# Kernel tuning notes

Hardware: AMD Instinct MI355X
Metric: run time of the kernel (lower is better)

The kernel has to match this reference:

```python
import jax, jax.numpy as jnp
import numpy as np

B, SQ, SK, D, H, DH = 4, 1024, 1024, 1024, 16, 64  # transform_units*head_units == 1024


def setup_inputs() -> dict:
    key = jax.random.key(0)
    ks = jax.random.split(key, 8)
    q = jax.random.normal(ks[0], (B, SQ, D), dtype=jnp.float32)
    v = jax.random.normal(ks[1], (B, SK, D), dtype=jnp.float32)
    q_mask = jax.random.randint(ks[2], (B, SQ), 0, 2).astype(bool).at[:, 0].set(True)
    v_mask = jax.random.randint(ks[3], (B, SK), 0, 2).astype(bool).at[:, 0].set(True)
    s = 0.02
    Wq = jax.random.normal(ks[4], (D, H * DH), dtype=jnp.float32) * s
    Wk = jax.random.normal(ks[5], (D, H * DH), dtype=jnp.float32) * s
    Wv = jax.random.normal(ks[6], (D, H * DH), dtype=jnp.float32) * s
    Wo = jax.random.normal(ks[7], (H * DH, D), dtype=jnp.float32) * s
    bq = jnp.zeros((H * DH,), jnp.float32)
    bk = jnp.zeros((H * DH,), jnp.float32)
    bv = jnp.zeros((H * DH,), jnp.float32)
    bo = jnp.zeros((D,), jnp.float32)
    return {"q": q, "v": v, "q_mask": q_mask, "v_mask": v_mask,
            "Wq": Wq, "bq": bq, "Wk": Wk, "bk": bk, "Wv": Wv, "bv": bv,
            "Wo": Wo, "bo": bo}


def reference(q, v, q_mask, v_mask, Wq, bq, Wk, bk, Wv, bv, Wo, bo):
    # k = v in the original module
    k = v
    # QKV projections; split-last-dim + batch-concat trick == reshape to heads
    Q = (q @ Wq + bq).reshape(B, SQ, H, DH)
    Kh = (k @ Wk + bk).reshape(B, SK, H, DH)
    V = (v @ Wv + bv).reshape(B, SK, H, DH)
    # Keras Attention: unscaled dot-product scores
    scores = jnp.einsum('bqhd,bkhd->bhqk', Q, Kh)  # [B,H,SQ,SK]
    scores = jnp.where(v_mask[:, None, None, :], scores, jnp.float32(-1e9))
    attn = jax.nn.softmax(scores, axis=-1)
    ctx = jnp.einsum('bhqk,bkhd->bqhd', attn, V).reshape(B, SQ, H * DH)
    # Keras Attention zeros masked query positions before output dense
    ctx = ctx * q_mask[:, :, None].astype(ctx.dtype)
    return ctx @ Wo + bo
```

## Files before the change

### kernel.cpp

```cpp
#include <hip/hip_runtime.h>
#include <hip/hip_fp16.h>

typedef __attribute__((ext_vector_type(8))) _Float16 f16x8;
typedef __attribute__((ext_vector_type(4))) float f32x4;

__device__ __forceinline__ void gload_lds16(const _Float16* g, _Float16* l) {
  __builtin_amdgcn_global_load_lds((const __attribute__((address_space(1))) void*)g,
                                   (__attribute__((address_space(3))) void*)l, 16, 0, 0);
}

__global__ __launch_bounds__(256) void prep_kernel(
    const float* __restrict__ q, const float* __restrict__ v,
    const float* __restrict__ W0, const float* __restrict__ W1,
    const float* __restrict__ W2, const float* __restrict__ W3,
    _Float16* __restrict__ q16, _Float16* __restrict__ v16,
    _Float16* __restrict__ T0, _Float16* __restrict__ T1,
    _Float16* __restrict__ T2, _Float16* __restrict__ T3) {
  __shared__ float tile[64 * 65];
  int tid = threadIdx.x, ybl = blockIdx.y;
  if (ybl < 16) {
    int i = (ybl * 256 + blockIdx.x) * 256 + tid;
    float4 fq = ((const float4*)q)[i];
    float4 fv = ((const float4*)v)[i];
    union { _Float16 h[4]; uint2 u; } oq, ov;
    oq.h[0] = (_Float16)fq.x; oq.h[1] = (_Float16)fq.y;
    oq.h[2] = (_Float16)fq.z; oq.h[3] = (_Float16)fq.w;
    ov.h[0] = (_Float16)fv.x; ov.h[1] = (_Float16)fv.y;
    ov.h[2] = (_Float16)fv.z; ov.h[3] = (_Float16)fv.w;
    *(uint2*)&q16[4 * (size_t)i] = oq.u;
    *(uint2*)&v16[4 * (size_t)i] = ov.u;
    return;
  }
  int z = ybl - 16;
  const float* W = (z == 0) ? W0 : (z == 1) ? W1 : (z == 2) ? W2 : W3;
  _Float16* T = (z == 0) ? T0 : (z == 1) ? T1 : (z == 2) ? T2 : T3;
  int bx = (blockIdx.x & 15) * 64, by = (blockIdx.x >> 4) * 64;
  for (int it = 0; it < 4; it++) {
    int lin = it * 256 + tid;
    int r = lin >> 4, q4 = (lin & 15) * 4;
    float4 f = *(const float4*)&W[(size_t)(by + r) * 1024 + bx + q4];
    tile[r * 65 + q4 + 0] = f.x;
    tile[r * 65 + q4 + 1] = f.y;
    tile[r * 65 + q4 + 2] = f.z;
    tile[r * 65 + q4 + 3] = f.w;
  }
  __syncthreads();
  for (int it = 0; it < 2; it++) {
    int lin = it * 256 + tid;
    int orow = lin >> 3, seg = (lin & 7) * 8;
    union { uint4 u; _Float16 h[8]; } o;
    for (int e = 0; e < 8; e++) o.h[e] = (_Float16)tile[(seg + e) * 65 + orow];
    *(uint4*)&T[(size_t)(bx + orow) * 1024 + by + seg] = o.u;
  }
}

__global__ __launch_bounds__(256, 3) void gemm_qkv_kernel(
    const _Float16* __restrict__ q16, const _Float16* __restrict__ v16,
    const _Float16* __restrict__ WqT, const _Float16* __restrict__ WkT,
    const _Float16* __restrict__ WvT,
    const float* __restrict__ bq, const float* __restrict__ bk, const float* __restrict__ bv,
    _Float16* __restrict__ Q16, _Float16* __restrict__ K16, _Float16* __restrict__ VT16) {
  int ord = blockIdx.x + (blockIdx.y << 3) + (blockIdx.z << 8);
  int wgid = (ord & 7) * 96 + (ord >> 3);
  int z = wgid >> 8;
  int rem = wgid & 255;
  int m0 = (rem >> 3) * 128, n0 = (rem & 7) * 128;

  const _Float16* A = (z == 0) ? q16 : v16;
  const _Float16* BT = (z == 0) ? WqT : ((z == 1) ? WkT : WvT);
  const float* bias = (z == 0) ? bq : ((z == 1) ? bk : bv);
  const int K = 1024;

  __shared__ _Float16 Alds[2][128 * 32];
  __shared__ _Float16 Blds[2][128 * 32];
  int tid = threadIdx.x, lane = tid & 63, w = tid >> 6;
  int c = lane & 15, g = lane >> 4;
  int wm = (w & 1) * 64, wn = (w >> 1) * 64;
  int rr = lane >> 2;
  int su = ((lane & 3) ^ (rr & 3)) * 8;

  const _Float16* gA[2]; const _Float16* gB[2]; int lo[2];
  for (int p = 0; p < 2; p++) {
    int row = w * 32 + p * 16 + rr;
    gA[p] = &A[(size_t)(m0 + row) * K + su];
    gB[p] = &BT[(size_t)(n0 + row) * K + su];
    lo[p] = (w * 32 + p * 16) * 32;
  }

  f32x4 acc[4][4];
  for (int i = 0; i < 4; i++)
    for (int j = 0; j < 4; j++)
      acc[i][j] = (f32x4){0.f, 0.f, 0.f, 0.f};

  for (int p = 0; p < 2; p++) {
    gload_lds16(gA[p], &Alds[0][lo[p]]);
    gload_lds16(gB[p], &Blds[0][lo[p]]);
  }
  __syncthreads();

  int xa = (c & 3) << 4;
  int cur = 0;
  for (int kt = 0; kt < 32; kt++) {
    if (kt + 1 < 32) {
      int nb = cur ^ 1;
      for (int p = 0; p < 2; p++) {
        gload_lds16(gA[p] + (kt + 1) * 32, &Alds[nb][lo[p]]);
        gload_lds16(gB[p] + (kt + 1) * 32, &Blds[nb][lo[p]]);
      }
    }
    const char* ab = (const char*)&Alds[cur][0];
    const char* bb = (const char*)&Blds[cur][0];
    f16x8 af[4], bf[4];
    for (int i = 0; i < 4; i++)
      af[i] = *(const f16x8*)(ab + (wm + i * 16 + c) * 64 + ((g * 16) ^ xa));
    for (int j = 0; j < 4; j++)
      bf[j] = *(const f16x8*)(bb + (wn + j * 16 + c) * 64 + ((g * 16) ^ xa));
    for (int i = 0; i < 4; i++)
      for (int j = 0; j < 4; j++)
        acc[i][j] = __builtin_amdgcn_mfma_f32_16x16x32_f16(af[i], bf[j], acc[i][j], 0, 0, 0);
    __syncthreads();
    cur ^= 1;
  }

  if (z < 2) {
    _Float16* C = (z == 0) ? Q16 : K16;
    for (int j = 0; j < 4; j++) {
      float bv_ = bias[n0 + wn + j * 16 + c];
      for (int i = 0; i < 4; i++) {
        int r = m0 + wm + i * 16 + g * 4;
        int cc = n0 + wn + j * 16 + c;
        for (int e = 0; e < 4; e++)
          C[(size_t)(r + e) * 1024 + cc] = (_Float16)(acc[i][j][e] + bv_);
      }
    }
  } else {
    for (int j = 0; j < 4; j++) {
      int cc = n0 + wn + j * 16 + c;
      float bv_ = bias[cc];
      int h_ = cc >> 6, dh = cc & 63;
      for (int i = 0; i < 4; i++) {
        int r = m0 + wm + i * 16 + g * 4;
        int b_ = r >> 10, key = r & 1023;
        union { uint2 u; _Float16 hh[4]; } o;
        for (int e = 0; e < 4; e++) o.hh[e] = (_Float16)(acc[i][j][e] + bv_);
        *(uint2*)&VT16[((size_t)((b_ * 16 + h_) * 64 + dh)) * 1024 + key] = o.u;
      }
    }
  }
}

__global__ __launch_bounds__(256, 2) void gemm_out_kernel(
    const _Float16* __restrict__ ctx16, const _Float16* __restrict__ WoT,
    const float* __restrict__ bo, float* __restrict__ out) {
  int ord = blockIdx.x + (blockIdx.y << 4);
  int wgid = (ord & 7) * 64 + (ord >> 3);
  int n0 = (wgid & 15) * 64, m0 = (wgid >> 4) * 128;
  const int K = 1024;
  __shared__ _Float16 Alds[2][128 * 32];
  __shared__ _Float16 Blds[2][64 * 32];
  int tid = threadIdx.x, lane = tid & 63, w = tid >> 6;
  int c = lane & 15, g = lane >> 4;
  int wm = (w & 1) * 64, wn = (w >> 1) * 32;
  int rr = lane >> 2;
  int su = ((lane & 3) ^ (rr & 3)) * 8;

  const _Float16* gA[2]; int laoff[2];
  for (int p = 0; p < 2; p++) {
    int row = w * 32 + p * 16 + rr;
    gA[p] = &ctx16[(size_t)(m0 + row) * K + su];
    laoff[p] = (w * 32 + p * 16) * 32;
  }
  const _Float16* gB; int lboff;
  {
    int row = w * 16 + rr;
    gB = &WoT[(size_t)(n0 + row) * K + su];
    lboff = (w * 16) * 32;
  }

  f32x4 acc[4][2];
  for (int i = 0; i < 4; i++)
    for (int j = 0; j < 2; j++)
      acc[i][j] = (f32x4){0.f, 0.f, 0.f, 0.f};

  for (int p = 0; p < 2; p++) gload_lds16(gA[p], &Alds[0][laoff[p]]);
  gload_lds16(gB, &Blds[0][lboff]);
  __syncthreads();

  int xa = (c & 3) << 4;
  int cur = 0;
  for (int kt = 0; kt < 32; kt++) {
    if (kt + 1 < 32) {
      int nb = cur ^ 1;
      for (int p = 0; p < 2; p++) gload_lds16(gA[p] + (kt + 1) * 32, &Alds[nb][laoff[p]]);
      gload_lds16(gB + (kt + 1) * 32, &Blds[nb][lboff]);
    }
    const char* ab = (const char*)&Alds[cur][0];
    const char* bb = (const char*)&Blds[cur][0];
    f16x8 af[4], bf[2];
    for (int i = 0; i < 4; i++)
      af[i] = *(const f16x8*)(ab + (wm + i * 16 + c) * 64 + ((g * 16) ^ xa));
    for (int j = 0; j < 2; j++)
      bf[j] = *(const f16x8*)(bb + (wn + j * 16 + c) * 64 + ((g * 16) ^ xa));
    for (int i = 0; i < 4; i++)
      for (int j = 0; j < 2; j++)
        acc[i][j] = __builtin_amdgcn_mfma_f32_16x16x32_f16(af[i], bf[j], acc[i][j], 0, 0, 0);
    __syncthreads();
    cur ^= 1;
  }
  for (int j = 0; j < 2; j++) {
    float bv_ = bo[n0 + wn + j * 16 + c];
    for (int i = 0; i < 4; i++) {
      int r = m0 + wm + i * 16 + g * 4;
      int cc = n0 + wn + j * 16 + c;
      for (int e = 0; e < 4; e++)
        out[(size_t)(r + e) * 1024 + cc] = acc[i][j][e] + bv_;
    }
  }
}

__global__ __launch_bounds__(256, 4) void attn_kernel(
    const _Float16* __restrict__ Q16, const _Float16* __restrict__ K16,
    const _Float16* __restrict__ VT16,
    const int* __restrict__ q_mask, const int* __restrict__ v_mask,
    _Float16* __restrict__ ctx16) {
  int ord = blockIdx.x + (blockIdx.y << 4) + (blockIdx.z << 8);
  int wgid = (ord & 7) * 128 + (ord >> 3);
  int qb = wgid & 15, h = (wgid >> 4) & 15, b = wgid >> 8;
  int tid = threadIdx.x, lane = tid & 63, w = tid >> 6;
  int c = lane & 15, g = lane >> 4;
  int lr = lane >> 3, ls = lane & 7;

  __shared__ _Float16 QP[64 * 64];
  __shared__ _Float16 Kl[2][64 * 64];
  __shared__ _Float16 Vl[2][64 * 64];

  const _Float16* Qg = Q16 + ((size_t)(b * 1024 + qb * 64)) * 1024 + h * 64;
  const _Float16* Kg = K16 + ((size_t)(b * 1024)) * 1024 + h * 64;
  const _Float16* Vg = VT16 + ((size_t)(b * 16 + h)) * 64 * 1024;

  int row0 = w * 16 + lr, row1 = row0 + 8;
  int kx = (ls ^ lr) * 8;
  int ch0 = w * 2, ch1 = w * 2 + 1;

  gload_lds16(Qg + (size_t)row0 * 1024 + kx, QP + ch0 * 512);
  gload_lds16(Qg + (size_t)row1 * 1024 + kx, QP + ch1 * 512);
  gload_lds16(Kg + (size_t)row0 * 1024 + kx, &Kl[0][ch0 * 512]);
  gload_lds16(Kg + (size_t)row1 * 1024 + kx, &Kl[0][ch1 * 512]);
  gload_lds16(Vg + (size_t)row0 * 1024 + kx, &Vl[0][ch0 * 512]);
  gload_lds16(Vg + (size_t)row1 * 1024 + kx, &Vl[0][ch1 * 512]);
  __syncthreads();

  f16x8 qf[2];
  {
    int row = w * 16 + c;
    const char* rb = (const char*)QP + row * 128;
    int x = (row & 7) << 4;
    qf[0] = *(const f16x8*)(rb + ((g * 16) ^ x));
    qf[1] = *(const f16x8*)(rb + ((64 + g * 16) ^ x));
    const _Float16 l2e = (_Float16)1.44269504f;
    for (int e = 0; e < 8; e++) { qf[0][e] *= l2e; qf[1][e] *= l2e; }
  }

  float lp[4] = {0.f, 0.f, 0.f, 0.f};
  f32x4 acc_o[4];
  for (int jd = 0; jd < 4; jd++) acc_o[jd] = (f32x4){0.f, 0.f, 0.f, 0.f};

  char* pb = (char*)QP;
  int cur = 0;
  const float REF = -23.0831222f;
  for (int kb = 0; kb < 16; kb++) {
    if (kb + 1 < 16) {
      int nb = cur ^ 1;
      const _Float16* kgs = Kg + (size_t)(kb + 1) * 64 * 1024;
      const _Float16* vgs = Vg + (kb + 1) * 64;
      gload_lds16(kgs + (size_t)row0 * 1024 + kx, &Kl[nb][ch0 * 512]);
      gload_lds16(kgs + (size_t)row1 * 1024 + kx, &Kl[nb][ch1 * 512]);
      gload_lds16(vgs + (size_t)row0 * 1024 + kx, &Vl[nb][ch0 * 512]);
      gload_lds16(vgs + (size_t)row1 * 1024 + kx, &Vl[nb][ch1 * 512]);
    }
    float madd[4];
    for (int j = 0; j < 4; j++)
      madd[j] = v_mask[b * 1024 + kb * 64 + j * 16 + c] ? REF : -1e30f;

    f32x4 s[4];
    const char* kbse = (const char*)&Kl[cur][0];
    for (int j = 0; j < 4; j++) {
      int row = j * 16 + c;
      const char* rb = kbse + row * 128;
      int x = (row & 7) << 4;
      f16x8 k0 = *(const f16x8*)(rb + ((g * 16) ^ x));
      f16x8 k1 = *(const f16x8*)(rb + ((64 + g * 16) ^ x));
      s[j] = (f32x4){0.f, 0.f, 0.f, 0.f};
      s[j] = __builtin_amdgcn_mfma_f32_16x16x32_f16(qf[0], k0, s[j], 0, 0, 0);
      s[j] = __builtin_amdgcn_mfma_f32_16x16x32_f16(qf[1], k1, s[j], 0, 0, 0);
    }

    for (int j = 0; j < 4; j++)
      for (int e = 0; e < 4; e++) {
        float p = exp2f(s[j][e] + madd[j]);
        s[j][e] = p;
        lp[e] += p;
      }

    for (int j = 0; j < 4; j++)
      for (int e = 0; e < 4; e++) {
        int prow = w * 16 + g * 4 + e;
        int pby = prow * 128 + (((j * 16 + c) * 2) ^ ((prow & 7) << 4));
        *(_Float16*)(pb + pby) = (_Float16)s[j][e];
      }
    asm volatile("s_waitcnt lgkmcnt(0)" ::: "memory");
    __builtin_amdgcn_sched_barrier(0);

    const char* vbse = (const char*)&Vl[cur][0];
    for (int ks = 0; ks < 2; ks++) {
      int prow = w * 16 + c;
      f16x8 pf = *(const f16x8*)(pb + prow * 128 +
                                 ((ks * 64 + g * 16) ^ ((prow & 7) << 4)));
      for (int jd = 0; jd < 4; jd++) {
        int vrow = jd * 16 + c;
        f16x8 vf = *(const f16x8*)(vbse + vrow * 128 +
                                   ((ks * 64 + g * 16) ^ ((vrow & 7) << 4)));
        acc_o[jd] = __builtin_amdgcn_mfma_f32_16x16x32_f16(pf, vf, acc_o[jd], 0, 0, 0);
      }
    }

    __syncthreads();
    cur ^= 1;
  }

  for (int e = 0; e < 4; e++) {
    lp[e] += __shfl_xor(lp[e], 1);
    lp[e] += __shfl_xor(lp[e], 2);
    lp[e] += __shfl_xor(lp[e], 4);
    lp[e] += __shfl_xor(lp[e], 8);
  }

  int qrow = b * 1024 + qb * 64 + w * 16 + g * 4;
  float inv[4];
  for (int e = 0; e < 4; e++) {
    float qm = q_mask[qrow + e] ? 1.0f : 0.0f;
    inv[e] = qm / lp[e];
  }
  _Float16* cb = ctx16 + ((size_t)qrow) * 1024 + h * 64;
  for (int jd = 0; jd < 4; jd++)
    for (int e = 0; e < 4; e++)
      cb[(size_t)e * 1024 + jd * 16 + c] = (_Float16)(acc_o[jd][e] * inv[e]);
}

extern "C" void kernel_launch(void* const* d_in, const int* in_sizes, int n_in,
                              void* d_out, int out_size, void* d_ws, size_t ws_size,
                              hipStream_t stream) {
  const float* q  = (const float*)d_in[0];
  const float* v  = (const float*)d_in[1];
  const int* q_mask = (const int*)d_in[2];
  const int* v_mask = (const int*)d_in[3];
  const float* Wq = (const float*)d_in[4];
  const float* bq = (const float*)d_in[5];
  const float* Wk = (const float*)d_in[6];
  const float* bk = (const float*)d_in[7];
  const float* Wv = (const float*)d_in[8];
  const float* bv = (const float*)d_in[9];
  const float* Wo = (const float*)d_in[10];
  const float* bo = (const float*)d_in[11];
  float* out = (float*)d_out;

  _Float16* ws = (_Float16*)d_ws;
  const size_t NE = (size_t)4 * 1024 * 1024;
  _Float16* q16   = ws;
  _Float16* v16   = ws + NE;
  _Float16* Q16   = ws + 2 * NE;
  _Float16* K16   = ws + 3 * NE;
  _Float16* VT16  = ws + 4 * NE;
  _Float16* ctx16 = ws + 5 * NE;
  _Float16* WqT   = ws + 6 * NE;
  _Float16* WkT   = WqT + 1024 * 1024;
  _Float16* WvT   = WkT + 1024 * 1024;
  _Float16* WoT   = WvT + 1024 * 1024;

  prep_kernel<<<dim3(256, 20), 256, 0, stream>>>(q, v, Wq, Wk, Wv, Wo,
                                                 q16, v16, WqT, WkT, WvT, WoT);
  gemm_qkv_kernel<<<dim3(8, 32, 3), 256, 0, stream>>>(q16, v16, WqT, WkT, WvT,
                                                      bq, bk, bv, Q16, K16, VT16);
  attn_kernel<<<dim3(16, 16, 4), 256, 0, stream>>>(Q16, K16, VT16, q_mask, v_mask, ctx16);
  gemm_out_kernel<<<dim3(16, 32), 256, 0, stream>>>(ctx16, WoT, bo, out);
}
```

Baseline: 201.7 us.

## Triple-buffer GEMM loads, double attention query tile, and pack key mask bits

Both GEMM kernels move from double to triple-buffered LDS staging, prefetching two k-steps ahead and using an explicit vmcnt wait plus a single barrier per iteration in place of two syncthreads. The attention kernel now handles 128 query rows per block, two 16-row tiles per wave, so each K/V fragment loaded from LDS feeds twice as many MFMAs. The key mask is packed into 64-bit words in the prep kernel, so the attention loop no longer reads per-key ints. The trade-off is higher LDS and register use, with changed launch bounds and occupancy targets, and a reliance on hand-counted vmcnt values being correct.

```diff
diff --git a/kernel.cpp b/kernel.cpp
--- a/kernel.cpp
+++ b/kernel.cpp
@@ -3,6 +3,7 @@
 
 typedef __attribute__((ext_vector_type(8))) _Float16 f16x8;
 typedef __attribute__((ext_vector_type(4))) float f32x4;
+typedef unsigned long long u64;
 
 __device__ __forceinline__ void gload_lds16(const _Float16* g, _Float16* l) {
   __builtin_amdgcn_global_load_lds((const __attribute__((address_space(1))) void*)g,
@@ -13,9 +14,11 @@
     const float* __restrict__ q, const float* __restrict__ v,
     const float* __restrict__ W0, const float* __restrict__ W1,
     const float* __restrict__ W2, const float* __restrict__ W3,
+    const int* __restrict__ v_mask,
     _Float16* __restrict__ q16, _Float16* __restrict__ v16,
     _Float16* __restrict__ T0, _Float16* __restrict__ T1,
-    _Float16* __restrict__ T2, _Float16* __restrict__ T3) {
+    _Float16* __restrict__ T2, _Float16* __restrict__ T3,
+    u64* __restrict__ mask_bits) {
   __shared__ float tile[64 * 65];
   int tid = threadIdx.x, ybl = blockIdx.y;
   if (ybl < 16) {
@@ -31,6 +34,16 @@
     *(uint2*)&v16[4 * (size_t)i] = ov.u;
     return;
   }
+  if (ybl == 20) {
+    if (blockIdx.x == 0 && tid < 64) {
+      int base = tid * 64;
+      u64 m = 0;
+      for (int k = 0; k < 64; k++)
+        m |= ((u64)(v_mask[base + k] != 0)) << k;
+      mask_bits[tid] = m;
+    }
+    return;
+  }
   int z = ybl - 16;
   const float* W = (z == 0) ? W0 : (z == 1) ? W1 : (z == 2) ? W2 : W3;
   _Float16* T = (z == 0) ? T0 : (z == 1) ? T1 : (z == 2) ? T2 : T3;
@@ -71,8 +84,8 @@
   const float* bias = (z == 0) ? bq : ((z == 1) ? bk : bv);
   const int K = 1024;
 
-  __shared__ _Float16 Alds[2][128 * 32];
-  __shared__ _Float16 Blds[2][128 * 32];
+  __shared__ _Float16 Alds[3][128 * 32];
+  __shared__ _Float16 Blds[3][128 * 32];
   int tid = threadIdx.x, lane = tid & 63, w = tid >> 6;
   int c = lane & 15, g = lane >> 4;
   int wm = (w & 1) * 64, wn = (w >> 1) * 64;
@@ -92,20 +105,24 @@
     for (int j = 0; j < 4; j++)
       acc[i][j] = (f32x4){0.f, 0.f, 0.f, 0.f};
 
-  for (int p = 0; p < 2; p++) {
-    gload_lds16(gA[p], &Alds[0][lo[p]]);
-    gload_lds16(gB[p], &Blds[0][lo[p]]);
-  }
-  __syncthreads();
+  for (int t = 0; t < 2; t++)
+    for (int p = 0; p < 2; p++) {
+      gload_lds16(gA[p] + t * 32, &Alds[t][lo[p]]);
+      gload_lds16(gB[p] + t * 32, &Blds[t][lo[p]]);
+    }
 
   int xa = (c & 3) << 4;
   int cur = 0;
   for (int kt = 0; kt < 32; kt++) {
-    if (kt + 1 < 32) {
-      int nb = cur ^ 1;
+    if (kt < 31) { asm volatile("s_waitcnt vmcnt(4)" ::: "memory"); }
+    else         { asm volatile("s_waitcnt vmcnt(0)" ::: "memory"); }
+    __builtin_amdgcn_s_barrier();
+    __builtin_amdgcn_sched_barrier(0);
+    if (kt + 2 < 32) {
+      int s2 = cur + 2; if (s2 >= 3) s2 -= 3;
       for (int p = 0; p < 2; p++) {
-        gload_lds16(gA[p] + (kt + 1) * 32, &Alds[nb][lo[p]]);
-        gload_lds16(gB[p] + (kt + 1) * 32, &Blds[nb][lo[p]]);
+        gload_lds16(gA[p] + (kt + 2) * 32, &Alds[s2][lo[p]]);
+        gload_lds16(gB[p] + (kt + 2) * 32, &Blds[s2][lo[p]]);
       }
     }
     const char* ab = (const char*)&Alds[cur][0];
@@ -118,8 +135,7 @@
     for (int i = 0; i < 4; i++)
       for (int j = 0; j < 4; j++)
         acc[i][j] = __builtin_amdgcn_mfma_f32_16x16x32_f16(af[i], bf[j], acc[i][j], 0, 0, 0);
-    __syncthreads();
-    cur ^= 1;
+    cur = (cur == 2) ? 0 : cur + 1;
   }
 
   if (z < 2) {
@@ -149,15 +165,15 @@
   }
 }
 
-__global__ __launch_bounds__(256, 2) void gemm_out_kernel(
+__global__ __launch_bounds__(256, 4) void gemm_out_kernel(
     const _Float16* __restrict__ ctx16, const _Float16* __restrict__ WoT,
     const float* __restrict__ bo, float* __restrict__ out) {
   int ord = blockIdx.x + (blockIdx.y << 4);
   int wgid = (ord & 7) * 64 + (ord >> 3);
   int n0 = (wgid & 15) * 64, m0 = (wgid >> 4) * 128;
   const int K = 1024;
-  __shared__ _Float16 Alds[2][128 * 32];
-  __shared__ _Float16 Blds[2][64 * 32];
+  __shared__ _Float16 Alds[3][128 * 32];
+  __shared__ _Float16 Blds[3][64 * 32];
   int tid = threadIdx.x, lane = tid & 63, w = tid >> 6;
   int c = lane & 15, g = lane >> 4;
   int wm = (w & 1) * 64, wn = (w >> 1) * 32;
@@ -182,17 +198,22 @@
     for (int j = 0; j < 2; j++)
       acc[i][j] = (f32x4){0.f, 0.f, 0.f, 0.f};
 
-  for (int p = 0; p < 2; p++) gload_lds16(gA[p], &Alds[0][laoff[p]]);
-  gload_lds16(gB, &Blds[0][lboff]);
-  __syncthreads();
+  for (int t = 0; t < 2; t++) {
+    for (int p = 0; p < 2; p++) gload_lds16(gA[p] + t * 32, &Alds[t][laoff[p]]);
+    gload_lds16(gB + t * 32, &Blds[t][lboff]);
+  }
 
   int xa = (c & 3) << 4;
   int cur = 0;
   for (int kt = 0; kt < 32; kt++) {
-    if (kt + 1 < 32) {
-      int nb = cur ^ 1;
-      for (int p = 0; p < 2; p++) gload_lds16(gA[p] + (kt + 1) * 32, &Alds[nb][laoff[p]]);
-      gload_lds16(gB + (kt + 1) * 32, &Blds[nb][lboff]);
+    if (kt < 31) { asm volatile("s_waitcnt vmcnt(3)" ::: "memory"); }
+    else         { asm volatile("s_waitcnt vmcnt(0)" ::: "memory"); }
+    __builtin_amdgcn_s_barrier();
+    __builtin_amdgcn_sched_barrier(0);
+    if (kt + 2 < 32) {
+      int s2 = cur + 2; if (s2 >= 3) s2 -= 3;
+      for (int p = 0; p < 2; p++) gload_lds16(gA[p] + (kt + 2) * 32, &Alds[s2][laoff[p]]);
+      gload_lds16(gB + (kt + 2) * 32, &Blds[s2][lboff]);
     }
     const char* ab = (const char*)&Alds[cur][0];
     const char* bb = (const char*)&Blds[cur][0];
@@ -204,8 +225,7 @@
     for (int i = 0; i < 4; i++)
       for (int j = 0; j < 2; j++)
         acc[i][j] = __builtin_amdgcn_mfma_f32_16x16x32_f16(af[i], bf[j], acc[i][j], 0, 0, 0);
-    __syncthreads();
-    cur ^= 1;
+    cur = (cur == 2) ? 0 : cur + 1;
   }
   for (int j = 0; j < 2; j++) {
     float bv_ = bo[n0 + wn + j * 16 + c];
@@ -218,52 +238,56 @@
   }
 }
 
-__global__ __launch_bounds__(256, 4) void attn_kernel(
+__global__ __launch_bounds__(256, 3) void attn_kernel(
     const _Float16* __restrict__ Q16, const _Float16* __restrict__ K16,
     const _Float16* __restrict__ VT16,
-    const int* __restrict__ q_mask, const int* __restrict__ v_mask,
+    const int* __restrict__ q_mask, const u64* __restrict__ mask_bits,
     _Float16* __restrict__ ctx16) {
-  int ord = blockIdx.x + (blockIdx.y << 4) + (blockIdx.z << 8);
-  int wgid = (ord & 7) * 128 + (ord >> 3);
-  int qb = wgid & 15, h = (wgid >> 4) & 15, b = wgid >> 8;
+  int qb = blockIdx.x, h = blockIdx.y, b = blockIdx.z;
   int tid = threadIdx.x, lane = tid & 63, w = tid >> 6;
   int c = lane & 15, g = lane >> 4;
   int lr = lane >> 3, ls = lane & 7;
 
-  __shared__ _Float16 QP[64 * 64];
+  __shared__ _Float16 QP[128 * 64];
   __shared__ _Float16 Kl[2][64 * 64];
   __shared__ _Float16 Vl[2][64 * 64];
 
-  const _Float16* Qg = Q16 + ((size_t)(b * 1024 + qb * 64)) * 1024 + h * 64;
+  const _Float16* Qg = Q16 + ((size_t)(b * 1024 + qb * 128)) * 1024 + h * 64;
   const _Float16* Kg = K16 + ((size_t)(b * 1024)) * 1024 + h * 64;
   const _Float16* Vg = VT16 + ((size_t)(b * 16 + h)) * 64 * 1024;
 
+  int kx = (ls ^ lr) * 8;
+  for (int p = 0; p < 4; p++) {
+    int ch = w * 4 + p;
+    gload_lds16(Qg + (size_t)(ch * 8 + lr) * 1024 + kx, QP + ch * 512);
+  }
   int row0 = w * 16 + lr, row1 = row0 + 8;
-  int kx = (ls ^ lr) * 8;
-  int ch0 = w * 2, ch1 = w * 2 + 1;
-
-  gload_lds16(Qg + (size_t)row0 * 1024 + kx, QP + ch0 * 512);
-  gload_lds16(Qg + (size_t)row1 * 1024 + kx, QP + ch1 * 512);
+  int ch0 = w * 2, ch1 = ch0 + 1;
   gload_lds16(Kg + (size_t)row0 * 1024 + kx, &Kl[0][ch0 * 512]);
   gload_lds16(Kg + (size_t)row1 * 1024 + kx, &Kl[0][ch1 * 512]);
   gload_lds16(Vg + (size_t)row0 * 1024 + kx, &Vl[0][ch0 * 512]);
   gload_lds16(Vg + (size_t)row1 * 1024 + kx, &Vl[0][ch1 * 512]);
   __syncthreads();
 
-  f16x8 qf[2];
+  f16x8 qf[2][2];
   {
-    int row = w * 16 + c;
-    const char* rb = (const char*)QP + row * 128;
-    int x = (row & 7) << 4;
-    qf[0] = *(const f16x8*)(rb + ((g * 16) ^ x));
-    qf[1] = *(const f16x8*)(rb + ((64 + g * 16) ^ x));
     const _Float16 l2e = (_Float16)1.44269504f;
-    for (int e = 0; e < 8; e++) { qf[0][e] *= l2e; qf[1][e] *= l2e; }
-  }
-
-  float lp[4] = {0.f, 0.f, 0.f, 0.f};
-  f32x4 acc_o[4];
-  for (int jd = 0; jd < 4; jd++) acc_o[jd] = (f32x4){0.f, 0.f, 0.f, 0.f};
+    for (int i = 0; i < 2; i++) {
+      int row = w * 32 + i * 16 + c;
+      const char* rb = (const char*)QP + row * 128;
+      int x = (c & 7) << 4;
+      qf[i][0] = *(const f16x8*)(rb + ((g * 16) ^ x));
+      qf[i][1] = *(const f16x8*)(rb + ((64 + g * 16) ^ x));
+      for (int e = 0; e < 8; e++) { qf[i][0][e] *= l2e; qf[i][1][e] *= l2e; }
+    }
+  }
+
+  float lp[2][4];
+  f32x4 acc_o[2][4];
+  for (int i = 0; i < 2; i++)
+    for (int e = 0; e < 4; e++) lp[i][e] = 0.f;
+  for (int i = 0; i < 2; i++)
+    for (int jd = 0; jd < 4; jd++) acc_o[i][jd] = (f32x4){0.f, 0.f, 0.f, 0.f};
 
   char* pb = (char*)QP;
   int cur = 0;
@@ -278,49 +302,58 @@
       gload_lds16(vgs + (size_t)row0 * 1024 + kx, &Vl[nb][ch0 * 512]);
       gload_lds16(vgs + (size_t)row1 * 1024 + kx, &Vl[nb][ch1 * 512]);
     }
+    u64 bits = mask_bits[b * 16 + kb];
     float madd[4];
     for (int j = 0; j < 4; j++)
-      madd[j] = v_mask[b * 1024 + kb * 64 + j * 16 + c] ? REF : -1e30f;
-
-    f32x4 s[4];
+      madd[j] = ((bits >> (unsigned)(j * 16 + c)) & 1ull) ? REF : -1e30f;
+
+    f16x8 kf[4][2];
     const char* kbse = (const char*)&Kl[cur][0];
     for (int j = 0; j < 4; j++) {
       int row = j * 16 + c;
       const char* rb = kbse + row * 128;
       int x = (row & 7) << 4;
-      f16x8 k0 = *(const f16x8*)(rb + ((g * 16) ^ x));
-      f16x8 k1 = *(const f16x8*)(rb + ((64 + g * 16) ^ x));
-      s[j] = (f32x4){0.f, 0.f, 0.f, 0.f};
-      s[j] = __builtin_amdgcn_mfma_f32_16x16x32_f16(qf[0], k0, s[j], 0, 0, 0);
-      s[j] = __builtin_amdgcn_mfma_f32_16x16x32_f16(qf[1], k1, s[j], 0, 0, 0);
-    }
-
-    for (int j = 0; j < 4; j++)
-      for (int e = 0; e < 4; e++) {
-        float p = exp2f(s[j][e] + madd[j]);
-        s[j][e] = p;
-        lp[e] += p;
-      }
-
-    for (int j = 0; j < 4; j++)
-      for (int e = 0; e < 4; e++) {
-        int prow = w * 16 + g * 4 + e;
-        int pby = prow * 128 + (((j * 16 + c) * 2) ^ ((prow & 7) << 4));
-        *(_Float16*)(pb + pby) = (_Float16)s[j][e];
-      }
+      kf[j][0] = *(const f16x8*)(rb + ((g * 16) ^ x));
+      kf[j][1] = *(const f16x8*)(rb + ((64 + g * 16) ^ x));
+    }
+
+    for (int i = 0; i < 2; i++) {
+      f32x4 s[4];
+      for (int j = 0; j < 4; j++) {
+        s[j] = (f32x4){0.f, 0.f, 0.f, 0.f};
+        s[j] = __builtin_amdgcn_mfma_f32_16x16x32_f16(qf[i][0], kf[j][0], s[j], 0, 0, 0);
+        s[j] = __builtin_amdgcn_mfma_f32_16x16x32_f16(qf[i][1], kf[j][1], s[j], 0, 0, 0);
+      }
+      for (int j = 0; j < 4; j++)
+        for (int e = 0; e < 4; e++) {
+          float p = exp2f(s[j][e] + madd[j]);
+          s[j][e] = p;
+          lp[i][e] += p;
+        }
+      for (int j = 0; j < 4; j++)
+        for (int e = 0; e < 4; e++) {
+          int prow = w * 32 + i * 16 + g * 4 + e;
+          int pby = prow * 128 + (((j * 16 + c) * 2) ^ ((prow & 7) << 4));
+          *(_Float16*)(pb + pby) = (_Float16)s[j][e];
+        }
+    }
     asm volatile("s_waitcnt lgkmcnt(0)" ::: "memory");
     __builtin_amdgcn_sched_barrier(0);
 
     const char* vbse = (const char*)&Vl[cur][0];
     for (int ks = 0; ks < 2; ks++) {
-      int prow = w * 16 + c;
-      f16x8 pf = *(const f16x8*)(pb + prow * 128 +
-                                 ((ks * 64 + g * 16) ^ ((prow & 7) << 4)));
+      f16x8 vf[4];
       for (int jd = 0; jd < 4; jd++) {
         int vrow = jd * 16 + c;
-        f16x8 vf = *(const f16x8*)(vbse + vrow * 128 +
-                                   ((ks * 64 + g * 16) ^ ((vrow & 7) << 4)));
-        acc_o[jd] = __builtin_amdgcn_mfma_f32_16x16x32_f16(pf, vf, acc_o[jd], 0, 0, 0);
+        vf[jd] = *(const f16x8*)(vbse + vrow * 128 +
+                                 ((ks * 64 + g * 16) ^ ((vrow & 7) << 4)));
+      }
+      for (int i = 0; i < 2; i++) {
+        int prow = w * 32 + i * 16 + c;
+        f16x8 pf = *(const f16x8*)(pb + prow * 128 +
+                                   ((ks * 64 + g * 16) ^ ((c & 7) << 4)));
+        for (int jd = 0; jd < 4; jd++)
+          acc_o[i][jd] = __builtin_amdgcn_mfma_f32_16x16x32_f16(pf, vf[jd], acc_o[i][jd], 0, 0, 0);
       }
     }
 
@@ -328,23 +361,26 @@
     cur ^= 1;
   }
 
-  for (int e = 0; e < 4; e++) {
-    lp[e] += __shfl_xor(lp[e], 1);
-    lp[e] += __shfl_xor(lp[e], 2);
-    lp[e] += __shfl_xor(lp[e], 4);
-    lp[e] += __shfl_xor(lp[e], 8);
-  }
-
-  int qrow = b * 1024 + qb * 64 + w * 16 + g * 4;
-  float inv[4];
-  for (int e = 0; e < 4; e++) {
-    float qm = q_mask[qrow + e] ? 1.0f : 0.0f;
-    inv[e] = qm / lp[e];
-  }
-  _Float16* cb = ctx16 + ((size_t)qrow) * 1024 + h * 64;
-  for (int jd = 0; jd < 4; jd++)
-    for (int e = 0; e < 4; e++)
-      cb[(size_t)e * 1024 + jd * 16 + c] = (_Float16)(acc_o[jd][e] * inv[e]);
+  for (int i = 0; i < 2; i++)
+    for (int e = 0; e < 4; e++) {
+      lp[i][e] += __shfl_xor(lp[i][e], 1);
+      lp[i][e] += __shfl_xor(lp[i][e], 2);
+      lp[i][e] += __shfl_xor(lp[i][e], 4);
+      lp[i][e] += __shfl_xor(lp[i][e], 8);
+    }
+
+  for (int i = 0; i < 2; i++) {
+    int qrow = b * 1024 + qb * 128 + w * 32 + i * 16 + g * 4;
+    float inv[4];
+    for (int e = 0; e < 4; e++) {
+      float qm = q_mask[qrow + e] ? 1.0f : 0.0f;
+      inv[e] = qm / lp[i][e];
+    }
+    _Float16* cb = ctx16 + ((size_t)qrow) * 1024 + h * 64;
+    for (int jd = 0; jd < 4; jd++)
+      for (int e = 0; e < 4; e++)
+        cb[(size_t)e * 1024 + jd * 16 + c] = (_Float16)(acc_o[i][jd][e] * inv[e]);
+  }
 }
 
 extern "C" void kernel_launch(void* const* d_in, const int* in_sizes, int n_in,
@@ -376,11 +412,12 @@
   _Float16* WkT   = WqT + 1024 * 1024;
   _Float16* WvT   = WkT + 1024 * 1024;
   _Float16* WoT   = WvT + 1024 * 1024;
-
-  prep_kernel<<<dim3(256, 20), 256, 0, stream>>>(q, v, Wq, Wk, Wv, Wo,
-                                                 q16, v16, WqT, WkT, WvT, WoT);
+  u64* mask_bits  = (u64*)(WoT + 1024 * 1024);
+
+  prep_kernel<<<dim3(256, 21), 256, 0, stream>>>(q, v, Wq, Wk, Wv, Wo, v_mask,
+                                                 q16, v16, WqT, WkT, WvT, WoT, mask_bits);
   gemm_qkv_kernel<<<dim3(8, 32, 3), 256, 0, stream>>>(q16, v16, WqT, WkT, WvT,
                                                       bq, bk, bv, Q16, K16, VT16);
-  attn_kernel<<<dim3(16, 16, 4), 256, 0, stream>>>(Q16, K16, VT16, q_mask, v_mask, ctx16);
+  attn_kernel<<<dim3(8, 16, 4), 256, 0, stream>>>(Q16, K16, VT16, q_mask, mask_bits, ctx16);
   gemm_out_kernel<<<dim3(16, 32), 256, 0, stream>>>(ctx16, WoT, bo, out);
 }
```

Result: slower. 208.0 us (+3.1%).
